# Kernel optimization log

Measured on AMD Instinct MI355X. Metric: run time of the kernel, lower is better.

The kernel has to match this reference:

```python
import jax, jax.numpy as jnp
import numpy as np

H = 16            # num_heads
SEG = 2048        # segment_size
DIL = 8           # dilation_rate
BLOCK_M = 64      # triton query block size (min(64, M_padded))


def setup_inputs() -> dict:
    key = jax.random.key(0)
    k1, k2, k3 = jax.random.split(key, 3)
    B, M, D = 2, 8192, 1024
    x = jax.random.normal(k1, (B, M, D), dtype=jnp.float32)
    Wqkv = jax.random.normal(k2, (3 * D, D), dtype=jnp.float32) * 0.02
    Wout = jax.random.normal(k3, (D, D), dtype=jnp.float32) * 0.02
    return {"x": x, "Wqkv": Wqkv, "Wout": Wout}


def reference(x, Wqkv, Wout):
    B, M, D = x.shape
    hd = D // H
    scale = hd ** -0.5
    S = M // SEG                      # number of segments (M is a multiple of SEG)
    Kn = SEG // DIL                   # dilated keys per segment
    nb = SEG // BLOCK_M               # query blocks per segment

    # qkv projection (torch Linear: x @ W^T), split into q,k,v: [B,H,M,hd]
    qkv = jnp.einsum('bmd,ed->bme', x, Wqkv).reshape(B, M, 3, H, hd)
    qkv = jnp.transpose(qkv, (2, 0, 3, 1, 4))
    q, k, v = qkv[0] * scale, qkv[1], qkv[2]

    # segment-local views
    q4 = q.reshape(B, H, S, SEG, hd)
    k4 = k.reshape(B, H, S, SEG, hd)[:, :, :, ::DIL]   # [B,H,S,Kn,hd] dilated keys
    v4 = v.reshape(B, H, S, SEG, hd)[:, :, :, ::DIL]

    # scores per segment: [B,H,S,SEG,Kn]
    scores = jnp.einsum('bhspd,bhskd->bhspk', q4, k4)
    # kernel normalization: per key j, subtract max over the 64-query block
    scores = scores.reshape(B, H, S, nb, BLOCK_M, Kn)
    c = jnp.max(scores, axis=4, keepdims=True)          # [B,H,S,nb,1,Kn]
    w = jnp.exp(scores - c)
    den = jnp.sum(w, axis=-1) + 1e-10                   # [B,H,S,nb,BLOCK_M]
    num = jnp.einsum('bhsnmk,bhskd->bhsnmd', w, v4)
    out = num / den[..., None]                          # [B,H,S,nb,BLOCK_M,hd]

    out = out.reshape(B, H, M, hd)
    out = jnp.transpose(out, (0, 2, 1, 3)).reshape(B, M, D)
    return jnp.einsum('bmd,ed->bme', out, Wout)
```

## Files before the change

kernel.cpp:

```cpp
#include <hip/hip_runtime.h>
#include <hip/hip_bf16.h>
#include <stdint.h>


typedef __attribute__((ext_vector_type(8))) short short8;
typedef __attribute__((ext_vector_type(4))) float f32x4;
typedef __attribute__((ext_vector_type(4))) unsigned short ushort4v;

#define DEVI static __device__ __forceinline__

DEVI unsigned short f2bf(float f) {
  union { float f; uint32_t u; } v; v.f = f;
  return (unsigned short)((v.u + 0x7FFFu + ((v.u >> 16) & 1u)) >> 16);
}

DEVI uint32_t pack_bf16(float lo, float hi) {
  return (uint32_t)f2bf(lo) | ((uint32_t)f2bf(hi) << 16);
}

DEVI void gload_lds16(const void* g, void* l) {
  __builtin_amdgcn_global_load_lds((const __attribute__((address_space(1))) void*)g,
                                   (__attribute__((address_space(3))) void*)l,
                                   16, 0, 0);
}

__global__ void cvt_kernel(const float* __restrict__ in, unsigned short* __restrict__ out, int n) {
  int i = (blockIdx.x * 256 + threadIdx.x) * 4;
  if (i >= n) return;
  float4 f = *(const float4*)(in + i);
  uint2 o;
  o.x = (uint32_t)f2bf(f.x) | ((uint32_t)f2bf(f.y) << 16);
  o.y = (uint32_t)f2bf(f.z) | ((uint32_t)f2bf(f.w) << 16);
  *(uint2*)(out + i) = o;
}

#define STAGE_A(bf, hf, kt) do { \
  gload_lds16(Abase + (long)((hf) * 128 + srow0) * 1024 + (kt) * 64 + scol0, &smA[bf][hf][se0]); \
  gload_lds16(Abase + (long)((hf) * 128 + srow1) * 1024 + (kt) * 64 + scol1, &smA[bf][hf][se1]); \
} while (0)
#define STAGE_B(bf, hf, kt) do { \
  gload_lds16(Bbase + (long)((hf) * 128 + srow0) * 1024 + (kt) * 64 + scol0, &smB[bf][hf][se0]); \
  gload_lds16(Bbase + (long)((hf) * 128 + srow1) * 1024 + (kt) * 64 + scol1, &smB[bf][hf][se1]); \
} while (0)

template<bool OUT_F32>
__global__ __launch_bounds__(512, 1) void gemm8p(
    const unsigned short* __restrict__ A, const unsigned short* __restrict__ B,
    void* __restrict__ Cv, float scale)
{
  __shared__ unsigned short smA[2][2][128 * 64];
  __shared__ unsigned short smB[2][2][128 * 64];
  const int tid = threadIdx.x;
  const int tm = blockIdx.x, tn = blockIdx.y;
  const int w = tid >> 6, lane = tid & 63;
  const int wm = w >> 2, wn = w & 3;
  const int lr = lane & 15, lq = lane >> 4;

  const int e0 = tid * 8,        e1 = (512 + tid) * 8;
  const int srow0 = e0 >> 6,     srow1 = e1 >> 6;
  const int sc0 = (e0 >> 3) & 7, sc1 = (e1 >> 3) & 7;
  const int scol0 = (sc0 ^ (srow0 & 7)) * 8, scol1 = (sc1 ^ (srow1 & 7)) * 8;
  const int se0 = e0, se1 = e1;

  const unsigned short* Abase = A + (long)tm * 256 * 1024;
  const unsigned short* Bbase = B + (long)tn * 256 * 1024;

  f32x4 acc[8][4] = {};
  short8 af[4][2];
  short8 bfr[2][2][2];

  STAGE_A(0, 0, 0); STAGE_B(0, 0, 0); STAGE_B(0, 1, 0); STAGE_A(0, 1, 0);
  asm volatile("s_waitcnt vmcnt(4)" ::: "memory");
  __builtin_amdgcn_s_barrier();
  asm volatile("" ::: "memory");

  for (int t = 0; t < 8; ++t) {
#pragma unroll
    for (int p = 0; p < 8; ++p) {
      const int o = p >> 2;
      const int q = p & 3;
      const int a = (p >> 1) & 1;
      const int b = a ^ (q & 1);

      if (q == 0 || q == 2) {
#pragma unroll
        for (int mi2 = 0; mi2 < 4; ++mi2) {
          int r = wm * 64 + mi2 * 16 + lr;
#pragma unroll
          for (int kk = 0; kk < 2; ++kk) {
            int kc = kk * 4 + lq;
            af[mi2][kk] = *(const short8*)&smA[o][a][r * 64 + ((kc ^ (r & 7)) * 8)];
          }
        }
      }
      if (q == 0 || q == 1) {
#pragma unroll
        for (int nj2 = 0; nj2 < 2; ++nj2) {
          int r = wn * 32 + nj2 * 16 + lr;
#pragma unroll
          for (int kk = 0; kk < 2; ++kk) {
            int kc = kk * 4 + lq;
            bfr[b][nj2][kk] = *(const short8*)&smB[o][b][r * 64 + ((kc ^ (r & 7)) * 8)];
          }
        }
      }

      switch (p) {
        case 0: STAGE_A(1, 0, 2 * t + 1); STAGE_B(1, 0, 2 * t + 1); break;
        case 2: STAGE_B(1, 1, 2 * t + 1); STAGE_A(1, 1, 2 * t + 1); break;
        case 4: if (t < 7) { STAGE_A(0, 0, 2 * t + 2); STAGE_B(0, 0, 2 * t + 2); } break;
        case 6: if (t < 7) { STAGE_B(0, 1, 2 * t + 2); STAGE_A(0, 1, 2 * t + 2); } break;
      }

      __builtin_amdgcn_s_barrier();
      if (q != 3) {
        asm volatile("s_waitcnt lgkmcnt(0)" ::: "memory");
        __builtin_amdgcn_sched_barrier(0);
      }

      __builtin_amdgcn_s_setprio(1);
#pragma unroll
      for (int kk = 0; kk < 2; ++kk)
#pragma unroll
        for (int mi2 = 0; mi2 < 4; ++mi2)
#pragma unroll
          for (int nj2 = 0; nj2 < 2; ++nj2)
            acc[a * 4 + mi2][b * 2 + nj2] = __builtin_amdgcn_mfma_f32_16x16x32_bf16(
                af[mi2][kk], bfr[b][nj2][kk], acc[a * 4 + mi2][b * 2 + nj2], 0, 0, 0);
      __builtin_amdgcn_s_setprio(0);

      if (t < 7) {
        if (p == 0 || p == 3 || p == 4 || p == 7)
          asm volatile("s_waitcnt vmcnt(4)" ::: "memory");
      } else {
        if (p == 0 || p == 3)  asm volatile("s_waitcnt vmcnt(4)" ::: "memory");
        else if (p == 4)       asm volatile("s_waitcnt vmcnt(0)" ::: "memory");
      }
      __builtin_amdgcn_s_barrier();
      asm volatile("" ::: "memory");
    }
  }

  const int row0 = tm * 256 + wm * 64 + lq * 4;
  const int col0 = tn * 256 + wn * 32 + lr;
#pragma unroll
  for (int mi = 0; mi < 8; ++mi) {
    int row = row0 + (mi & 3) * 16 + (mi >> 2) * 128;
#pragma unroll
    for (int nj = 0; nj < 4; ++nj) {
      int col = col0 + (nj & 1) * 16 + (nj >> 1) * 128;
#pragma unroll
      for (int rr = 0; rr < 4; ++rr) {
        float v = acc[mi][nj][rr] * scale;
        long off = (long)(row + rr) * 1024 + col;
        if (OUT_F32) ((float*)Cv)[off] = v;
        else         ((unsigned short*)Cv)[off] = f2bf(v);
      }
    }
  }
}

template<int EPI>
__global__ __launch_bounds__(256, 2) void gemm_bt(
    const unsigned short* __restrict__ A, const unsigned short* __restrict__ B,
    void* __restrict__ Cv, unsigned short* __restrict__ Cv2,
    float scale, long a_row_stride, int ldc, int K)
{
  __shared__ unsigned short smA[128 * 64];
  __shared__ unsigned short smB[128 * 64];
  const int tid = threadIdx.x;
  const int tm = blockIdx.x, tn = blockIdx.y;
  const int w = tid >> 6, lane = tid & 63;
  const int wr = (w >> 1) * 64, wc = (w & 1) * 64;
  const int lr = lane & 15, lq = lane >> 4;

  int se[4], srow[4], scol[4];
#pragma unroll
  for (int i = 0; i < 4; ++i) {
    int e = (i * 256 + tid) * 8;
    int r = e >> 6;
    int cc = (e >> 3) & 7;
    se[i] = e; srow[i] = r; scol[i] = (cc ^ (r & 7)) * 8;
  }

  f32x4 acc[4][4] = {};

  for (int kt = 0; kt < K / 64; ++kt) {
    if (kt) __syncthreads();
#pragma unroll
    for (int i = 0; i < 4; ++i)
      gload_lds16(A + (long)(tm * 128 + srow[i]) * a_row_stride + kt * 64 + scol[i], &smA[se[i]]);
#pragma unroll
    for (int i = 0; i < 4; ++i)
      gload_lds16(B + (long)(tn * 128 + srow[i]) * K + kt * 64 + scol[i], &smB[se[i]]);
    __syncthreads();

#pragma unroll
    for (int kk = 0; kk < 2; ++kk) {
      int kc = kk * 4 + lq;
      short8 af[4], bfm[4];
#pragma unroll
      for (int i = 0; i < 4; ++i) {
        int row = wr + i * 16 + lr;
        af[i] = *(const short8*)&smA[row * 64 + ((kc ^ (row & 7)) * 8)];
      }
#pragma unroll
      for (int j = 0; j < 4; ++j) {
        int row = wc + j * 16 + lr;
        bfm[j] = *(const short8*)&smB[row * 64 + ((kc ^ (row & 7)) * 8)];
      }
#pragma unroll
      for (int i = 0; i < 4; ++i)
#pragma unroll
        for (int j = 0; j < 4; ++j)
          acc[i][j] = __builtin_amdgcn_mfma_f32_16x16x32_bf16(af[i], bfm[j], acc[i][j], 0, 0, 0);
    }
  }

  if (EPI == 2 && tn >= 8) {
    const int fbase = (tn - 8) * 128 + wc;
#pragma unroll
    for (int ip = 0; ip < 4; ip += 2) {
      int t0 = tm * 128 + wr + ip * 16 + lq * 4;
      int seg = t0 >> 8;
      int ts  = t0 & 255;
      int c32 = (ts >> 5) * 16 + (ts & 15);
#pragma unroll
      for (int j = 0; j < 4; ++j) {
        int f = fbase + j * 16 + lr;
        uint32_t* rp = (uint32_t*)&Cv2[((long)(seg * 1024 + f)) * 256];
        uint4 U;
        U.x = pack_bf16(acc[ip][j][0] * scale, acc[ip + 1][j][0] * scale);
        U.y = pack_bf16(acc[ip][j][1] * scale, acc[ip + 1][j][1] * scale);
        U.z = pack_bf16(acc[ip][j][2] * scale, acc[ip + 1][j][2] * scale);
        U.w = pack_bf16(acc[ip][j][3] * scale, acc[ip + 1][j][3] * scale);
        *(uint4*)&rp[c32] = U;
      }
    }
    return;
  }

#pragma unroll
  for (int i = 0; i < 4; ++i) {
    int rg0 = tm * 128 + wr + i * 16 + lq * 4;
#pragma unroll
    for (int j = 0; j < 4; ++j) {
      int cg = tn * 128 + wc + j * 16 + lr;
#pragma unroll
      for (int r = 0; r < 4; ++r) {
        float v = acc[i][j][r] * scale;
        long off = (long)(rg0 + r) * ldc + cg;
        if (EPI == 0) ((float*)Cv)[off] = v;
        else          ((unsigned short*)Cv)[off] = f2bf(v);
      }
    }
  }
}

__global__ __launch_bounds__(512, 2) void attn_kernel(
    const unsigned short* __restrict__ qb,
    const unsigned short* __restrict__ kb,
    const unsigned short* __restrict__ vtb,
    unsigned short* __restrict__ attout)
{
  __shared__ unsigned short v_t[64 * 256];
  __shared__ uint32_t w32[8][64][20];

  const int u = (blockIdx.x & 7) * 64 + (blockIdx.x >> 3);
  const int quarter = u & 3, h = (u >> 2) & 15, s = (u >> 6) & 3, b = u >> 8;
  const int tid = threadIdx.x, w = tid >> 6, lane = tid & 63;
  const int lr = lane & 15, lq = lane >> 4;
  const long qrow0 = (long)b * 8192 + s * 2048 + quarter * 512 + w * 64;
  const int hc = h * 64;

  const unsigned short* kbase = kb + ((long)(b * 4 + s) * 256) * 1024 + hc;
  const unsigned short* vbase = vtb + ((long)(b * 4 + s) * 1024 + hc) * 256;

#pragma unroll
  for (int it = 0; it < 4; ++it) {
    int e = (it * 512 + tid) * 8;
    int f = e >> 8;
    int ch = (e >> 3) & 31;
    gload_lds16(vbase + (long)f * 256 + ((ch ^ (f & 7)) * 8), &v_t[e]);
  }

  const unsigned short* qbase = qb + qrow0 * 1024 + hc;
  short8 aq[4][2];
#pragma unroll
  for (int i = 0; i < 4; ++i)
#pragma unroll
    for (int kk = 0; kk < 2; ++kk)
      aq[i][kk] = *(const short8*)&qbase[(i * 16 + lr) * 1024 + (kk * 4 + lq) * 8];

  __syncthreads();

  short8 ones;
#pragma unroll
  for (int e = 0; e < 8; ++e) ones[e] = (short)0x3F80;

  uint32_t (*wsl)[20] = w32[w];

  f32x4 acc_pv[4][4] = {};
  f32x4 acc_den[4] = {};
  short8 bk0[2][2], bk1[2][2];
  f32x4 sA[4][2], sB[4][2];

#define LOADK(BK, CC) do { \
  _Pragma("unroll") for (int j = 0; j < 2; ++j) \
    _Pragma("unroll") for (int kk = 0; kk < 2; ++kk) \
      BK[j][kk] = *(const short8*)&kbase[(long)((CC) * 32 + j * 16 + lr) * 1024 + (kk * 4 + lq) * 8]; \
} while (0)

#define QKT(S, BK) do { \
  _Pragma("unroll") for (int i = 0; i < 4; ++i) \
    _Pragma("unroll") for (int j = 0; j < 2; ++j) { \
      f32x4 z = {0.f, 0.f, 0.f, 0.f}; S[i][j] = z; } \
  _Pragma("unroll") for (int kk = 0; kk < 2; ++kk) \
    _Pragma("unroll") for (int i = 0; i < 4; ++i) \
      _Pragma("unroll") for (int j = 0; j < 2; ++j) \
        S[i][j] = __builtin_amdgcn_mfma_f32_16x16x32_bf16(aq[i][kk], BK[j][kk], S[i][j], 0, 0, 0); \
} while (0)

#define SOFTPV(S, CC) do { \
  float c0 = -3.4e38f, c1 = -3.4e38f; \
  _Pragma("unroll") for (int i = 0; i < 4; ++i) \
    _Pragma("unroll") for (int r = 0; r < 4; ++r) { \
      c0 = fmaxf(c0, S[i][0][r]); c1 = fmaxf(c1, S[i][1][r]); } \
  c0 = fmaxf(c0, __shfl_xor(c0, 16)); c0 = fmaxf(c0, __shfl_xor(c0, 32)); \
  c1 = fmaxf(c1, __shfl_xor(c1, 16)); c1 = fmaxf(c1, __shfl_xor(c1, 32)); \
  _Pragma("unroll") for (int i = 0; i < 4; ++i) \
    _Pragma("unroll") for (int r = 0; r < 4; ++r) { \
      int qq = i * 16 + lq * 4 + r; \
      wsl[qq][lr] = pack_bf16(__expf(S[i][0][r] - c0), __expf(S[i][1][r] - c1)); } \
  short8 av_[4]; \
  _Pragma("unroll") for (int ct = 0; ct < 4; ++ct) { \
    int frow = ct * 16 + lr; \
    av_[ct] = *(const short8*)&v_t[frow * 256 + ((((CC) * 4 + lq) ^ (frow & 7)) << 3)]; } \
  _Pragma("unroll") for (int qi = 0; qi < 4; ++qi) { \
    short8 bw = *(const short8*)&wsl[qi * 16 + lr][lq * 4]; \
    acc_den[qi] = __builtin_amdgcn_mfma_f32_16x16x32_bf16(ones, bw, acc_den[qi], 0, 0, 0); \
    _Pragma("unroll") for (int ct = 0; ct < 4; ++ct) \
      acc_pv[qi][ct] = __builtin_amdgcn_mfma_f32_16x16x32_bf16(av_[ct], bw, acc_pv[qi][ct], 0, 0, 0); } \
} while (0)

  LOADK(bk0, 0);
  LOADK(bk1, 1);
  QKT(sA, bk0);

  LOADK(bk0, 2); QKT(sB, bk1); SOFTPV(sA, 0);
  LOADK(bk1, 3); QKT(sA, bk0); SOFTPV(sB, 1);
  LOADK(bk0, 4); QKT(sB, bk1); SOFTPV(sA, 2);
  LOADK(bk1, 5); QKT(sA, bk0); SOFTPV(sB, 3);
  LOADK(bk0, 6); QKT(sB, bk1); SOFTPV(sA, 4);
  LOADK(bk1, 7); QKT(sA, bk0); SOFTPV(sB, 5);
                 QKT(sB, bk1); SOFTPV(sA, 6);
                               SOFTPV(sB, 7);

#pragma unroll
  for (int qi = 0; qi < 4; ++qi) {
    float inv = 1.0f / (acc_den[qi][0] + 1e-10f);
    long orow = (qrow0 + qi * 16 + lr) * 1024 + hc;
#pragma unroll
    for (int ct = 0; ct < 4; ++ct) {
      ushort4v p;
#pragma unroll
      for (int r = 0; r < 4; ++r) p[r] = f2bf(acc_pv[qi][ct][r] * inv);
      *(ushort4v*)&attout[orow + ct * 16 + lq * 4] = p;
    }
  }
}

extern "C" void kernel_launch(void* const* d_in, const int* in_sizes, int n_in,
                              void* d_out, int out_size, void* d_ws, size_t ws_size,
                              hipStream_t stream) {
  (void)in_sizes; (void)n_in; (void)out_size; (void)ws_size;
  const float* x    = (const float*)d_in[0];
  const float* Wqkv = (const float*)d_in[1];
  const float* Wout = (const float*)d_in[2];
  float* out = (float*)d_out;
  char* ws = (char*)d_ws;

  unsigned short* xb     = (unsigned short*)(ws);
  unsigned short* attout = (unsigned short*)(ws);
  unsigned short* wqkvb  = (unsigned short*)(ws + 33554432);
  unsigned short* woutb  = (unsigned short*)(ws + 39845888);
  unsigned short* qbuf   = (unsigned short*)(ws + 41943040);
  unsigned short* kbuf   = (unsigned short*)(ws + 75497472);
  unsigned short* vtb    = (unsigned short*)(ws + 79691776);

  cvt_kernel<<<16384, 256, 0, stream>>>(x, xb, 16777216);
  cvt_kernel<<<3072, 256, 0, stream>>>(Wqkv, wqkvb, 3 * 1024 * 1024);
  cvt_kernel<<<1024, 256, 0, stream>>>(Wout, woutb, 1024 * 1024);

  gemm8p<false><<<dim3(64, 4), 512, 0, stream>>>(xb, wqkvb, (void*)qbuf, 0.125f);
  gemm_bt<2><<<dim3(16, 16), 256, 0, stream>>>(
      xb, wqkvb + 1024 * 1024, (void*)kbuf, vtb, 1.0f, 8192, 1024, 1024);

  attn_kernel<<<512, 512, 0, stream>>>(qbuf, kbuf, vtb, attout);

  gemm8p<true><<<dim3(64, 4), 512, 0, stream>>>(attout, woutb, (void*)out, 1.0f);
}
```

Before: 165.8 us.

## Fuse fp32-to-bf16 conversion of x into GEMM A-tile staging

Removes the separate x conversion kernel. The Q GEMM and the K/V GEMM now read fp32 x directly, convert it in registers and store bf16 into LDS. The old direct global-to-LDS loads for A are replaced by register loads, which changes the vmcnt accounting and may weaken the async pipelining. It also swaps round-to-nearest-even bf16 packing for a cheaper round-half-up pack in the attention softmax and the output store, a slight numeric change.

```diff
diff --git a/kernel.cpp b/kernel.cpp
--- a/kernel.cpp
+++ b/kernel.cpp
@@ -16,12 +16,24 @@
 
 DEVI uint32_t pack_bf16(float lo, float hi) {
   return (uint32_t)f2bf(lo) | ((uint32_t)f2bf(hi) << 16);
+}
+
+DEVI uint32_t pack_hu(float lo, float hi) {
+  union { float f; uint32_t u; } a, b; a.f = lo; b.f = hi;
+  return ((a.u + 0x8000u) >> 16) | ((b.u + 0x8000u) & 0xFFFF0000u);
 }
 
 DEVI void gload_lds16(const void* g, void* l) {
   __builtin_amdgcn_global_load_lds((const __attribute__((address_space(1))) void*)g,
                                    (__attribute__((address_space(3))) void*)l,
                                    16, 0, 0);
+}
+
+DEVI uint4 cvt8_hu(float4 x, float4 y) {
+  uint4 r;
+  r.x = pack_hu(x.x, x.y); r.y = pack_hu(x.z, x.w);
+  r.z = pack_hu(y.x, y.y); r.w = pack_hu(y.z, y.w);
+  return r;
 }
 
 __global__ void cvt_kernel(const float* __restrict__ in, unsigned short* __restrict__ out, int n) {
@@ -34,18 +46,9 @@
   *(uint2*)(out + i) = o;
 }
 
-#define STAGE_A(bf, hf, kt) do { \
-  gload_lds16(Abase + (long)((hf) * 128 + srow0) * 1024 + (kt) * 64 + scol0, &smA[bf][hf][se0]); \
-  gload_lds16(Abase + (long)((hf) * 128 + srow1) * 1024 + (kt) * 64 + scol1, &smA[bf][hf][se1]); \
-} while (0)
-#define STAGE_B(bf, hf, kt) do { \
-  gload_lds16(Bbase + (long)((hf) * 128 + srow0) * 1024 + (kt) * 64 + scol0, &smB[bf][hf][se0]); \
-  gload_lds16(Bbase + (long)((hf) * 128 + srow1) * 1024 + (kt) * 64 + scol1, &smB[bf][hf][se1]); \
-} while (0)
-
-template<bool OUT_F32>
+template<bool A_F32, bool OUT_F32>
 __global__ __launch_bounds__(512, 1) void gemm8p(
-    const unsigned short* __restrict__ A, const unsigned short* __restrict__ B,
+    const void* __restrict__ Av, const unsigned short* __restrict__ B,
     void* __restrict__ Cv, float scale)
 {
   __shared__ unsigned short smA[2][2][128 * 64];
@@ -62,15 +65,36 @@
   const int scol0 = (sc0 ^ (srow0 & 7)) * 8, scol1 = (sc1 ^ (srow1 & 7)) * 8;
   const int se0 = e0, se1 = e1;
 
-  const unsigned short* Abase = A + (long)tm * 256 * 1024;
+  const unsigned short* Ab16 = (const unsigned short*)Av + (long)tm * 256 * 1024;
+  const float*          Ab32 = (const float*)Av + (long)tm * 256 * 1024;
   const unsigned short* Bbase = B + (long)tn * 256 * 1024;
+
+  auto stage_a = [&](int bf, int hf, int kt) {
+    if constexpr (A_F32) {
+      const float* s0 = Ab32 + (long)(hf * 128 + srow0) * 1024 + kt * 64 + scol0;
+      const float* s1 = Ab32 + (long)(hf * 128 + srow1) * 1024 + kt * 64 + scol1;
+      float4 x0 = *(const float4*)s0, y0 = *(const float4*)(s0 + 4);
+      float4 x1 = *(const float4*)s1, y1 = *(const float4*)(s1 + 4);
+      *(uint4*)&smA[bf][hf][se0] = cvt8_hu(x0, y0);
+      *(uint4*)&smA[bf][hf][se1] = cvt8_hu(x1, y1);
+    } else {
+      gload_lds16(Ab16 + (long)(hf * 128 + srow0) * 1024 + kt * 64 + scol0, &smA[bf][hf][se0]);
+      gload_lds16(Ab16 + (long)(hf * 128 + srow1) * 1024 + kt * 64 + scol1, &smA[bf][hf][se1]);
+    }
+  };
+  auto stage_b = [&](int bf, int hf, int kt) {
+    gload_lds16(Bbase + (long)(hf * 128 + srow0) * 1024 + kt * 64 + scol0, &smB[bf][hf][se0]);
+    gload_lds16(Bbase + (long)(hf * 128 + srow1) * 1024 + kt * 64 + scol1, &smB[bf][hf][se1]);
+  };
 
   f32x4 acc[8][4] = {};
   short8 af[4][2];
   short8 bfr[2][2][2];
 
-  STAGE_A(0, 0, 0); STAGE_B(0, 0, 0); STAGE_B(0, 1, 0); STAGE_A(0, 1, 0);
-  asm volatile("s_waitcnt vmcnt(4)" ::: "memory");
+  stage_b(0, 0, 0); stage_b(0, 1, 0);
+  stage_a(0, 0, 0); stage_a(0, 1, 0);
+  if constexpr (A_F32) asm volatile("s_waitcnt vmcnt(2)" ::: "memory");
+  else                 asm volatile("s_waitcnt vmcnt(4)" ::: "memory");
   __builtin_amdgcn_s_barrier();
   asm volatile("" ::: "memory");
 
@@ -106,10 +130,10 @@
       }
 
       switch (p) {
-        case 0: STAGE_A(1, 0, 2 * t + 1); STAGE_B(1, 0, 2 * t + 1); break;
-        case 2: STAGE_B(1, 1, 2 * t + 1); STAGE_A(1, 1, 2 * t + 1); break;
-        case 4: if (t < 7) { STAGE_A(0, 0, 2 * t + 2); STAGE_B(0, 0, 2 * t + 2); } break;
-        case 6: if (t < 7) { STAGE_B(0, 1, 2 * t + 2); STAGE_A(0, 1, 2 * t + 2); } break;
+        case 0: stage_b(1, 0, 2 * t + 1); stage_a(1, 0, 2 * t + 1); break;
+        case 2: stage_b(1, 1, 2 * t + 1); stage_a(1, 1, 2 * t + 1); break;
+        case 4: if (t < 7) { stage_b(0, 0, 2 * t + 2); stage_a(0, 0, 2 * t + 2); } break;
+        case 6: if (t < 7) { stage_b(0, 1, 2 * t + 2); stage_a(0, 1, 2 * t + 2); } break;
       }
 
       __builtin_amdgcn_s_barrier();
@@ -130,11 +154,17 @@
       __builtin_amdgcn_s_setprio(0);
 
       if (t < 7) {
-        if (p == 0 || p == 3 || p == 4 || p == 7)
-          asm volatile("s_waitcnt vmcnt(4)" ::: "memory");
+        if (p == 0 || p == 3 || p == 4 || p == 7) {
+          if constexpr (A_F32) asm volatile("s_waitcnt vmcnt(2)" ::: "memory");
+          else                 asm volatile("s_waitcnt vmcnt(4)" ::: "memory");
+        }
       } else {
-        if (p == 0 || p == 3)  asm volatile("s_waitcnt vmcnt(4)" ::: "memory");
-        else if (p == 4)       asm volatile("s_waitcnt vmcnt(0)" ::: "memory");
+        if (p == 0 || p == 3) {
+          if constexpr (A_F32) asm volatile("s_waitcnt vmcnt(2)" ::: "memory");
+          else                 asm volatile("s_waitcnt vmcnt(4)" ::: "memory");
+        } else if (p == 4) {
+          asm volatile("s_waitcnt vmcnt(0)" ::: "memory");
+        }
       }
       __builtin_amdgcn_s_barrier();
       asm volatile("" ::: "memory");
@@ -162,7 +192,7 @@
 
 template<int EPI>
 __global__ __launch_bounds__(256, 2) void gemm_bt(
-    const unsigned short* __restrict__ A, const unsigned short* __restrict__ B,
+    const float* __restrict__ A, const unsigned short* __restrict__ B,
     void* __restrict__ Cv, unsigned short* __restrict__ Cv2,
     float scale, long a_row_stride, int ldc, int K)
 {
@@ -188,8 +218,11 @@
   for (int kt = 0; kt < K / 64; ++kt) {
     if (kt) __syncthreads();
 #pragma unroll
-    for (int i = 0; i < 4; ++i)
-      gload_lds16(A + (long)(tm * 128 + srow[i]) * a_row_stride + kt * 64 + scol[i], &smA[se[i]]);
+    for (int i = 0; i < 4; ++i) {
+      const float* s = A + (long)(tm * 128 + srow[i]) * a_row_stride + kt * 64 + scol[i];
+      float4 x0 = *(const float4*)s, y0 = *(const float4*)(s + 4);
+      *(uint4*)&smA[se[i]] = cvt8_hu(x0, y0);
+    }
 #pragma unroll
     for (int i = 0; i < 4; ++i)
       gload_lds16(B + (long)(tn * 128 + srow[i]) * K + kt * 64 + scol[i], &smB[se[i]]);
@@ -331,7 +364,7 @@
   _Pragma("unroll") for (int i = 0; i < 4; ++i) \
     _Pragma("unroll") for (int r = 0; r < 4; ++r) { \
       int qq = i * 16 + lq * 4 + r; \
-      wsl[qq][lr] = pack_bf16(__expf(S[i][0][r] - c0), __expf(S[i][1][r] - c1)); } \
+      wsl[qq][lr] = pack_hu(__expf(S[i][0][r] - c0), __expf(S[i][1][r] - c1)); } \
   short8 av_[4]; \
   _Pragma("unroll") for (int ct = 0; ct < 4; ++ct) { \
     int frow = ct * 16 + lr; \
@@ -362,10 +395,10 @@
     long orow = (qrow0 + qi * 16 + lr) * 1024 + hc;
 #pragma unroll
     for (int ct = 0; ct < 4; ++ct) {
-      ushort4v p;
-#pragma unroll
-      for (int r = 0; r < 4; ++r) p[r] = f2bf(acc_pv[qi][ct][r] * inv);
-      *(ushort4v*)&attout[orow + ct * 16 + lq * 4] = p;
+      uint2 p;
+      p.x = pack_hu(acc_pv[qi][ct][0] * inv, acc_pv[qi][ct][1] * inv);
+      p.y = pack_hu(acc_pv[qi][ct][2] * inv, acc_pv[qi][ct][3] * inv);
+      *(uint2*)&attout[orow + ct * 16 + lq * 4] = p;
     }
   }
 }
@@ -380,7 +413,6 @@
   float* out = (float*)d_out;
   char* ws = (char*)d_ws;
 
-  unsigned short* xb     = (unsigned short*)(ws);
   unsigned short* attout = (unsigned short*)(ws);
   unsigned short* wqkvb  = (unsigned short*)(ws + 33554432);
   unsigned short* woutb  = (unsigned short*)(ws + 39845888);
@@ -388,15 +420,16 @@
   unsigned short* kbuf   = (unsigned short*)(ws + 75497472);
   unsigned short* vtb    = (unsigned short*)(ws + 79691776);
 
-  cvt_kernel<<<16384, 256, 0, stream>>>(x, xb, 16777216);
   cvt_kernel<<<3072, 256, 0, stream>>>(Wqkv, wqkvb, 3 * 1024 * 1024);
   cvt_kernel<<<1024, 256, 0, stream>>>(Wout, woutb, 1024 * 1024);
 
-  gemm8p<false><<<dim3(64, 4), 512, 0, stream>>>(xb, wqkvb, (void*)qbuf, 0.125f);
+  gemm8p<true, false><<<dim3(64, 4), 512, 0, stream>>>(
+      (const void*)x, wqkvb, (void*)qbuf, 0.125f);
   gemm_bt<2><<<dim3(16, 16), 256, 0, stream>>>(
-      xb, wqkvb + 1024 * 1024, (void*)kbuf, vtb, 1.0f, 8192, 1024, 1024);
+      x, wqkvb + 1024 * 1024, (void*)kbuf, vtb, 1.0f, 8192, 1024, 1024);
 
   attn_kernel<<<512, 512, 0, stream>>>(qbuf, kbuf, vtb, attout);
 
-  gemm8p<true><<<dim3(64, 4), 512, 0, stream>>>(attout, woutb, (void*)out, 1.0f);
-}
+  gemm8p<false, true><<<dim3(64, 4), 512, 0, stream>>>(
+      (const void*)attout, woutb, (void*)out, 1.0f);
+}
```

Measured after the change: 174.5 us. 1.05x slower.

## Read V directly from global in attention, drop LDS staging and barrier

Applied to the files above, without the earlier changes.

The attention kernel no longer stages the transposed V tile into shared memory with a block-wide barrier; each wave loads its V fragments straight from global (L2-resident) memory inside the softmax/PV step. This frees 32KB of LDS per block and removes the __syncthreads, which could raise occupancy and let waves start immediately. It also replaces round-to-nearest-even bf16 conversion with a cheaper round-half-up packing and rewrites the max reduction as a tree. The cost is repeated global loads of V by all 8 waves, and the rounding differs slightly from before.

```diff
diff --git a/kernel.cpp b/kernel.cpp
--- a/kernel.cpp
+++ b/kernel.cpp
@@ -5,7 +5,6 @@
 
 typedef __attribute__((ext_vector_type(8))) short short8;
 typedef __attribute__((ext_vector_type(4))) float f32x4;
-typedef __attribute__((ext_vector_type(4))) unsigned short ushort4v;
 
 #define DEVI static __device__ __forceinline__
 
@@ -16,6 +15,11 @@
 
 DEVI uint32_t pack_bf16(float lo, float hi) {
   return (uint32_t)f2bf(lo) | ((uint32_t)f2bf(hi) << 16);
+}
+
+DEVI uint32_t pack_hu(float lo, float hi) {
+  union { float f; uint32_t u; } a, b; a.f = lo; b.f = hi;
+  return ((a.u + 0x8000u) >> 16) | ((b.u + 0x8000u) & 0xFFFF0000u);
 }
 
 DEVI void gload_lds16(const void* g, void* l) {
@@ -263,7 +267,6 @@
     const unsigned short* __restrict__ vtb,
     unsigned short* __restrict__ attout)
 {
-  __shared__ unsigned short v_t[64 * 256];
   __shared__ uint32_t w32[8][64][20];
 
   const int u = (blockIdx.x & 7) * 64 + (blockIdx.x >> 3);
@@ -276,14 +279,6 @@
   const unsigned short* kbase = kb + ((long)(b * 4 + s) * 256) * 1024 + hc;
   const unsigned short* vbase = vtb + ((long)(b * 4 + s) * 1024 + hc) * 256;
 
-#pragma unroll
-  for (int it = 0; it < 4; ++it) {
-    int e = (it * 512 + tid) * 8;
-    int f = e >> 8;
-    int ch = (e >> 3) & 31;
-    gload_lds16(vbase + (long)f * 256 + ((ch ^ (f & 7)) * 8), &v_t[e]);
-  }
-
   const unsigned short* qbase = qb + qrow0 * 1024 + hc;
   short8 aq[4][2];
 #pragma unroll
@@ -291,8 +286,6 @@
 #pragma unroll
     for (int kk = 0; kk < 2; ++kk)
       aq[i][kk] = *(const short8*)&qbase[(i * 16 + lr) * 1024 + (kk * 4 + lq) * 8];
-
-  __syncthreads();
 
   short8 ones;
 #pragma unroll
@@ -322,20 +315,24 @@
 } while (0)
 
 #define SOFTPV(S, CC) do { \
-  float c0 = -3.4e38f, c1 = -3.4e38f; \
-  _Pragma("unroll") for (int i = 0; i < 4; ++i) \
-    _Pragma("unroll") for (int r = 0; r < 4; ++r) { \
-      c0 = fmaxf(c0, S[i][0][r]); c1 = fmaxf(c1, S[i][1][r]); } \
+   \
+  short8 av_[4]; \
+  _Pragma("unroll") for (int ct = 0; ct < 4; ++ct) \
+    av_[ct] = *(const short8*)&vbase[(ct * 16 + lr) * 256 + ((CC) * 4 + lq) * 8]; \
+   \
+  float p0[4], p1[4]; \
+  _Pragma("unroll") for (int i = 0; i < 4; ++i) { \
+    p0[i] = fmaxf(fmaxf(S[i][0][0], S[i][0][1]), fmaxf(S[i][0][2], S[i][0][3])); \
+    p1[i] = fmaxf(fmaxf(S[i][1][0], S[i][1][1]), fmaxf(S[i][1][2], S[i][1][3])); \
+  } \
+  float c0 = fmaxf(fmaxf(p0[0], p0[1]), fmaxf(p0[2], p0[3])); \
+  float c1 = fmaxf(fmaxf(p1[0], p1[1]), fmaxf(p1[2], p1[3])); \
   c0 = fmaxf(c0, __shfl_xor(c0, 16)); c0 = fmaxf(c0, __shfl_xor(c0, 32)); \
   c1 = fmaxf(c1, __shfl_xor(c1, 16)); c1 = fmaxf(c1, __shfl_xor(c1, 32)); \
   _Pragma("unroll") for (int i = 0; i < 4; ++i) \
     _Pragma("unroll") for (int r = 0; r < 4; ++r) { \
       int qq = i * 16 + lq * 4 + r; \
-      wsl[qq][lr] = pack_bf16(__expf(S[i][0][r] - c0), __expf(S[i][1][r] - c1)); } \
-  short8 av_[4]; \
-  _Pragma("unroll") for (int ct = 0; ct < 4; ++ct) { \
-    int frow = ct * 16 + lr; \
-    av_[ct] = *(const short8*)&v_t[frow * 256 + ((((CC) * 4 + lq) ^ (frow & 7)) << 3)]; } \
+      wsl[qq][lr] = pack_hu(__expf(S[i][0][r] - c0), __expf(S[i][1][r] - c1)); } \
   _Pragma("unroll") for (int qi = 0; qi < 4; ++qi) { \
     short8 bw = *(const short8*)&wsl[qi * 16 + lr][lq * 4]; \
     acc_den[qi] = __builtin_amdgcn_mfma_f32_16x16x32_bf16(ones, bw, acc_den[qi], 0, 0, 0); \
@@ -362,10 +359,10 @@
     long orow = (qrow0 + qi * 16 + lr) * 1024 + hc;
 #pragma unroll
     for (int ct = 0; ct < 4; ++ct) {
-      ushort4v p;
-#pragma unroll
-      for (int r = 0; r < 4; ++r) p[r] = f2bf(acc_pv[qi][ct][r] * inv);
-      *(ushort4v*)&attout[orow + ct * 16 + lq * 4] = p;
+      uint2 p;
+      p.x = pack_hu(acc_pv[qi][ct][0] * inv, acc_pv[qi][ct][1] * inv);
+      p.y = pack_hu(acc_pv[qi][ct][2] * inv, acc_pv[qi][ct][3] * inv);
+      *(uint2*)&attout[orow + ct * 16 + lq * 4] = p;
     }
   }
 }
```

New measurement: 170.1 us. 2.6% more time.
